# Kernel optimization log

Measured on AMD Instinct MI355X. Metric: run time of the kernel, lower is better.

The kernel has to match this reference:

```python
import jax, jax.numpy as jnp
import numpy as np

B, H, W, S, C = 16, 128, 128, 4, 64
SC = S * C
SK_ITERS, SK_EPS = 20, 1e-6


def setup_inputs() -> dict:
    key = jax.random.key(0)
    ks = jax.random.split(key, 12)
    x = jax.random.normal(ks[0], (B, H, W, S, C), dtype=jnp.float32)
    # torch Linear weights are [out, in], kaiming-uniform-ish scale ~ 1/sqrt(in)
    w_pre = jax.random.normal(ks[1], (S, SC), dtype=jnp.float32) / np.sqrt(SC)
    w_post = jax.random.normal(ks[2], (S, SC), dtype=jnp.float32) / np.sqrt(SC)
    w_res = jax.random.normal(ks[3], (S * S, SC), dtype=jnp.float32) / np.sqrt(SC)
    b_pre = jax.random.normal(ks[4], (1, S), dtype=jnp.float32) * 0.01
    b_res = jax.random.normal(ks[5], (S * S,), dtype=jnp.float32) * 0.01
    b_post = jax.random.normal(ks[6], (1, S), dtype=jnp.float32) * 0.01
    alpha_pre = jax.random.normal(ks[7], (1,), dtype=jnp.float32) * 0.01
    alpha_res = jax.random.normal(ks[8], (1,), dtype=jnp.float32) * 0.01
    alpha_post = jax.random.normal(ks[9], (1,), dtype=jnp.float32) * 0.01
    rms_w = jnp.ones((SC,), dtype=jnp.float32)
    # conv kernel HWIO for 3x3 same-padded Conv2d(C, C, bias=False)
    conv_w = jax.random.normal(ks[10], (3, 3, C, C), dtype=jnp.float32) / np.sqrt(9 * C)
    return {"x": x, "w_pre": w_pre, "w_post": w_post, "w_res": w_res,
            "b_pre": b_pre, "b_res": b_res, "b_post": b_post,
            "alpha_pre": alpha_pre, "alpha_res": alpha_res, "alpha_post": alpha_post,
            "rms_w": rms_w, "conv_w": conv_w}


def _sinkhorn(h_tilde):
    # h_tilde: [B,H,W,S,S]; stable softmax-style shift then 20 row/col rescales
    h = h_tilde - h_tilde.max(axis=(-2, -1), keepdims=True)
    h = jnp.exp(h)
    def body(_, h):
        h = h / (h.sum(axis=-2, keepdims=True) + SK_EPS)
        h = h / (h.sum(axis=-1, keepdims=True) + SK_EPS)
        return h
    return jax.lax.fori_loop(0, SK_ITERS, body, h)


def reference(x, w_pre, w_post, w_res, b_pre, b_res, b_post,
              alpha_pre, alpha_res, alpha_post, rms_w, conv_w):
    s = b_pre.shape[-1]
    x_arrow = x.reshape(*x.shape[:-2], -1)           # [B,H,W,S*C]
    eps = jnp.finfo(x.dtype).eps                     # torch RMSNorm default eps
    x_norm = x_arrow * jax.lax.rsqrt(jnp.mean(x_arrow * x_arrow, axis=-1, keepdims=True) + eps)
    x_norm = x_norm * rms_w

    h_tilde_pre = alpha_pre * (x_norm @ w_pre.T) + b_pre          # [B,H,W,S]
    h_tilde_post = alpha_post * (x_norm @ w_post.T) + b_post       # [B,H,W,S]
    h_tilde_res = alpha_res * (x_norm @ w_res.T).reshape(*x.shape[:-2], s, s) \
                  + b_res.reshape(s, s)                            # [B,H,W,S,S]

    h_pre = jax.nn.sigmoid(h_tilde_pre)                            # [B,H,W,S]
    h_res = _sinkhorn(h_tilde_res)                                 # [B,H,W,S,S]
    h_post = 2.0 * jax.nn.sigmoid(h_tilde_post)                    # [B,H,W,S]

    # x_pre = h_pre @ x (pre-mix across streams) -> [B,H,W,C]
    x_pre = jnp.einsum('bhws,bhwsc->bhwc', h_pre, x)
    # layer: Conv2d(C,C,3,padding=1,bias=False), applied in NHWC directly
    layer_out = jax.lax.conv_general_dilated(
        x_pre, conv_w, window_strides=(1, 1), padding='SAME',
        dimension_numbers=('NHWC', 'HWIO', 'NHWC'))                # [B,H,W,C]

    out = jnp.einsum('bhwst,bhwtc->bhwsc', h_res, x) \
          + h_post[..., :, None] * layer_out[..., None, :]         # [B,H,W,S,C]
    return out
```

## Files before the change

kernel.cpp:

```cpp
#include <hip/hip_runtime.h>
#include <cstdint>
#include <cstring>

typedef unsigned int u32;
typedef unsigned short u16;
typedef __attribute__((ext_vector_type(8))) __bf16 bf16x8;
typedef __attribute__((ext_vector_type(4))) float f32x4;

#define DEV static __device__ __forceinline__

DEV float bf2f(u16 v){ u32 u = ((u32)v)<<16; float f; __builtin_memcpy(&f,&u,4); return f; }
DEV u16 f2bf(float f){ u32 u; __builtin_memcpy(&u,&f,4); u32 r = u + 0x7fffu + ((u>>16)&1u); return (u16)(r>>16); }
DEV void unpk(u32 v, float& lo, float& hi){
  u32 a = v<<16; u32 b = v & 0xffff0000u;
  __builtin_memcpy(&lo,&a,4); __builtin_memcpy(&hi,&b,4);
}
DEV u32 pk2(float lo, float hi){ return (u32)f2bf(lo) | (((u32)f2bf(hi))<<16); }
DEV float fsigm(float x){ return __builtin_amdgcn_rcpf(1.f + __expf(-x)); }
DEV f32x4 MFMA16(uint4 a, uint4 b, f32x4 c){
  return __builtin_amdgcn_mfma_f32_16x16x32_bf16(
      __builtin_bit_cast(bf16x8, a), __builtin_bit_cast(bf16x8, b), c, 0, 0, 0);
}

DEV bool detect_bf16(const void* rmsw){ return ((const u16*)rmsw)[0] == 0x3F80u; }

DEV u32 rnd1(u32 f){ return (f + 0x7fffu + ((f>>16)&1u)) >> 16; }
DEV u32 rnd2(u32 lo, u32 hi){ return rnd1(lo) | (rnd1(hi)<<16); }

DEV uint4 load8(const void* p, size_t idx8, bool bf){
  if (bf) return ((const uint4*)p)[idx8];
  const uint4* q = (const uint4*)p;
  uint4 a = q[2*idx8], b = q[2*idx8+1];
  return make_uint4(rnd2(a.x,a.y), rnd2(a.z,a.w), rnd2(b.x,b.y), rnd2(b.z,b.w));
}
DEV void store8(void* p, size_t idx8, bool bf, const float* v){
  if (bf){
    ((uint4*)p)[idx8] = make_uint4(pk2(v[0],v[1]),pk2(v[2],v[3]),pk2(v[4],v[5]),pk2(v[6],v[7]));
  } else {
    float4* q = (float4*)p;
    q[2*idx8]   = make_float4(v[0],v[1],v[2],v[3]);
    q[2*idx8+1] = make_float4(v[4],v[5],v[6],v[7]);
  }
}
DEV float ldsc(const void* p, int i, bool bf){
  return bf ? bf2f(((const u16*)p)[i]) : ((const float*)p)[i];
}

__global__ __launch_bounds__(256) void prepack_kernel(
    const void* __restrict__ wpre, const void* __restrict__ wpost,
    const void* __restrict__ wres, const void* __restrict__ rmsw,
    const void* __restrict__ convw, u16* __restrict__ wsW, u16* __restrict__ wsC)
{
  const bool bf = detect_bf16(rmsw);
  int tid = blockIdx.x*256 + threadIdx.x;
  if (tid < 8192){
    int i = tid & 7, lane = (tid>>3)&63, nt = (tid>>9)&1, kk = tid>>10;
    int j = nt*16 + (lane&15);
    int k = kk*32 + ((lane>>4)<<3) + i;
    float v = 0.f;
    if (j < 4)       v = ldsc(wpre, j*256+k, bf);
    else if (j < 8)  v = ldsc(wpost, (j-4)*256+k, bf);
    else if (j < 24) v = ldsc(wres, (j-8)*256+k, bf);
    v *= ldsc(rmsw, k, bf);
    wsW[tid] = f2bf(v);
  }
  if (tid < 36864){
    int i = tid & 7, lane = (tid>>3)&63, nt = (tid>>9)&3, kk = tid>>11;
    int co = nt*16 + (lane&15);
    int k = kk*32 + ((lane>>4)<<3) + i;
    wsC[tid] = f2bf(ldsc(convw, k*64+co, bf));
  }
}

__global__ __launch_bounds__(256,2) void mHC_fused_kernel(
    const void* __restrict__ x,
    const void* __restrict__ bpre, const void* __restrict__ bres, const void* __restrict__ bpost,
    const void* __restrict__ apre, const void* __restrict__ ares, const void* __restrict__ apost,
    const void* __restrict__ rmsw,
    const u16* __restrict__ wsW, const u16* __restrict__ wsC,
    void* __restrict__ out)
{
  __shared__ __align__(16) u16 s_xpre[18*18*68];
  __shared__ __align__(16) u16 s_h[256*20];
  __shared__ __align__(16) u16 s_hpre[4][64];
  __shared__ __align__(16) u16 s_L[4][16*68];

  const bool bf = detect_bf16(rmsw);
  const int tid = threadIdx.x;
  const int wave = tid>>6, lane = tid&63;
  const int mm = lane&15, q = lane>>4;
  const int blk = blockIdx.x;
  const int bimg = blk>>6, ty = (blk>>3)&7, tx = blk&7;
  const size_t xb8 = (size_t)bimg*16384*32;
  const int gy0 = ty*16-1, gx0 = tx*16-1;

  const float a_pre = ldsc(apre,0,bf), a_res = ldsc(ares,0,bf), a_post = ldsc(apost,0,bf);
  const float al0 = (mm<4)? a_pre : (mm<8)? a_post : a_res;
  const float bi0 = (mm<4)? ldsc(bpre,mm,bf) : (mm<8)? ldsc(bpost,mm-4,bf) : ldsc(bres,mm-8,bf);
  const float al1 = a_res;
  const float bi1 = (mm<8)? ldsc(bres,mm+8,bf) : 0.f;

  const uint4* wWv = reinterpret_cast<const uint4*>(wsW);
  const uint4* wCv = reinterpret_cast<const uint4*>(wsC);

  for (int pass = wave; pass < 21; pass += 4){
    const int P  = pass*16 + mm;
    const int ey = P/18, ex = P - ey*18;
    const int gy = gy0+ey, gx = gx0+ex;
    const bool inimg = (P<324) && ((u32)gy < 128u) && ((u32)gx < 128u);
    const size_t p8 = xb8 + (size_t)(u32)(gy*128 + gx)*32;

    uint4 A[8];
    #pragma unroll
    for (int kk=0;kk<8;kk++){
      uint4 v = make_uint4(0u,0u,0u,0u);
      if (inimg) v = load8(x, p8 + kk*4+q, bf);
      A[kk] = v;
    }
    float ssq = 0.f;
    #pragma unroll
    for (int kk=0;kk<8;kk++){
      const u32 vv[4] = {A[kk].x,A[kk].y,A[kk].z,A[kk].w};
      #pragma unroll
      for (int w2=0;w2<4;w2++){ float lo,hi; unpk(vv[w2],lo,hi);
        ssq = __builtin_fmaf(lo,lo,ssq); ssq = __builtin_fmaf(hi,hi,ssq); }
    }
    ssq += __shfl_xor(ssq,16);
    ssq += __shfl_xor(ssq,32);
    const float scale = __builtin_amdgcn_rsqf(ssq*(1.f/256.f) + 1.1920928955078125e-07f);
    float rs[4];
    #pragma unroll
    for (int r=0;r<4;r++) rs[r] = __shfl(scale, q*4+r);

    f32x4 D0 = {0.f,0.f,0.f,0.f}, D1 = {0.f,0.f,0.f,0.f};
    #pragma unroll
    for (int kk=0;kk<8;kk++){
      D0 = MFMA16(A[kk], wWv[(kk*2+0)*64+lane], D0);
      D1 = MFMA16(A[kk], wWv[(kk*2+1)*64+lane], D1);
    }
    #pragma unroll
    for (int r=0;r<4;r++){
      const float ht0 = __builtin_fmaf(al0*rs[r], D0[r], bi0);
      const float ht1 = __builtin_fmaf(al1*rs[r], D1[r], bi1);
      const int Pr = pass*16 + q*4 + r;
      const int eyr = Pr/18, exr = Pr - eyr*18;
      if (mm < 4) s_hpre[wave][(q*4+r)*4+mm] = f2bf(fsigm(ht0));
      const bool intr = (Pr<324) && (eyr>=1) && (eyr<=16) && (exr>=1) && (exr<=16);
      if (intr){
        const int pid = (eyr-1)*16 + (exr-1);
        if (mm < 8) s_h[pid*20 + mm+8] = f2bf(ht1);
        else        s_h[pid*20 + mm-8] = f2bf(ht0);
        if (mm>=4 && mm<8) s_h[pid*20 + 12 + mm] = f2bf(2.f*fsigm(ht0));
      }
    }
    __builtin_amdgcn_wave_barrier();
    if (P < 324){
      float hp[4];
      { const uint2 hv = *reinterpret_cast<const uint2*>(&s_hpre[wave][mm*4]);
        unpk(hv.x, hp[0], hp[1]); unpk(hv.y, hp[2], hp[3]); }
      float xa[8] = {0,0,0,0,0,0,0,0}, xb[8] = {0,0,0,0,0,0,0,0};
      #pragma unroll
      for (int kk=0;kk<8;kk++){
        const float h = hp[kk>>1];
        const u32 vv[4] = {A[kk].x,A[kk].y,A[kk].z,A[kk].w};
        #pragma unroll
        for (int w2=0;w2<4;w2++){
          float lo,hi; unpk(vv[w2],lo,hi);
          if (kk&1){ xb[2*w2]  =__builtin_fmaf(h,lo,xb[2*w2]);  xb[2*w2+1]=__builtin_fmaf(h,hi,xb[2*w2+1]); }
          else     { xa[2*w2]  =__builtin_fmaf(h,lo,xa[2*w2]);  xa[2*w2+1]=__builtin_fmaf(h,hi,xa[2*w2+1]); }
        }
      }
      const int pix = ey*18+ex;
      uint2* dA = reinterpret_cast<uint2*>(&s_xpre[pix*68 + 8*q]);
      dA[0] = make_uint2(pk2(xa[0],xa[1]), pk2(xa[2],xa[3]));
      dA[1] = make_uint2(pk2(xa[4],xa[5]), pk2(xa[6],xa[7]));
      uint2* dB = reinterpret_cast<uint2*>(&s_xpre[pix*68 + 32 + 8*q]);
      dB[0] = make_uint2(pk2(xb[0],xb[1]), pk2(xb[2],xb[3]));
      dB[1] = make_uint2(pk2(xb[4],xb[5]), pk2(xb[6],xb[7]));
    }
    __builtin_amdgcn_wave_barrier();
  }
  __syncthreads();

  {
    const int p = tid;
    float h[16];
    const uint2* h2 = reinterpret_cast<const uint2*>(&s_h[p*20]);
    #pragma unroll
    for (int e=0;e<4;e++){ const uint2 v = h2[e];
      unpk(v.x,h[4*e],h[4*e+1]); unpk(v.y,h[4*e+2],h[4*e+3]); }
    float mx = h[0];
    #pragma unroll
    for (int e=1;e<16;e++) mx = fmaxf(mx,h[e]);
    #pragma unroll
    for (int e=0;e<16;e++) h[e] = __expf(h[e]-mx);
    for (int it=0; it<20; ++it){
      #pragma unroll
      for (int t=0;t<4;t++){
        const float rc = __builtin_amdgcn_rcpf((h[t]+h[4+t])+(h[8+t]+h[12+t]) + 1e-6f);
        h[t]*=rc; h[4+t]*=rc; h[8+t]*=rc; h[12+t]*=rc;
      }
      #pragma unroll
      for (int s=0;s<4;s++){
        const float rc = __builtin_amdgcn_rcpf((h[4*s]+h[4*s+1])+(h[4*s+2]+h[4*s+3]) + 1e-6f);
        h[4*s]*=rc; h[4*s+1]*=rc; h[4*s+2]*=rc; h[4*s+3]*=rc;
      }
    }
    uint2* hw = reinterpret_cast<uint2*>(&s_h[p*20]);
    #pragma unroll
    for (int e=0;e<4;e++) hw[e] = make_uint2(pk2(h[4*e],h[4*e+1]), pk2(h[4*e+2],h[4*e+3]));
  }
  __syncthreads();

  for (int i=0;i<4;i++){
    const int py = wave*4+i;
    f32x4 D[4];
    #pragma unroll
    for (int nt=0;nt<4;nt++) D[nt] = (f32x4){0.f,0.f,0.f,0.f};
    #pragma unroll
    for (int kk=0;kk<18;kk++){
      const int tq  = 4*kk+q;
      const int tap = tq>>3;
      const int ci0 = (tq&7)*8;
      const int dy = tap/3, dx = tap-3*dy;
      const int pix = (py+dy)*18 + (mm+dx);
      const uint2* a2 = reinterpret_cast<const uint2*>(&s_xpre[pix*68 + ci0]);
      const uint2 alo = a2[0], ahi = a2[1];
      const uint4 av = make_uint4(alo.x, alo.y, ahi.x, ahi.y);
      #pragma unroll
      for (int nt=0;nt<4;nt++)
        D[nt] = MFMA16(av, wCv[(kk*4+nt)*64+lane], D[nt]);
    }
    __builtin_amdgcn_wave_barrier();
    #pragma unroll
    for (int nt=0;nt<4;nt++)
      #pragma unroll
      for (int r=0;r<4;r++)
        s_L[wave][(q*4+r)*68 + nt*16 + mm] = f2bf(D[nt][r]);
    __builtin_amdgcn_wave_barrier();

    const int gy = ty*16+py, gx = tx*16+mm;
    const size_t p8 = xb8 + (size_t)(gy*128+gx)*32;
    uint4 A[8];
    #pragma unroll
    for (int kk=0;kk<8;kk++) A[kk] = load8(x, p8 + kk*4+q, bf);
    float xa[4][8], xb[4][8];
    #pragma unroll
    for (int t=0;t<4;t++){
      const u32 va[4] = {A[2*t].x,A[2*t].y,A[2*t].z,A[2*t].w};
      const u32 vb[4] = {A[2*t+1].x,A[2*t+1].y,A[2*t+1].z,A[2*t+1].w};
      #pragma unroll
      for (int w2=0;w2<4;w2++){
        unpk(va[w2], xa[t][2*w2], xa[t][2*w2+1]);
        unpk(vb[w2], xb[t][2*w2], xb[t][2*w2+1]);
      }
    }
    const int pid = py*16+mm;
    float hr[16], hpo[4];
    {
      const uint2* h2 = reinterpret_cast<const uint2*>(&s_h[pid*20]);
      #pragma unroll
      for (int e=0;e<4;e++){ const uint2 v = h2[e];
        unpk(v.x,hr[4*e],hr[4*e+1]); unpk(v.y,hr[4*e+2],hr[4*e+3]); }
      const uint2 v4 = h2[4];
      unpk(v4.x,hpo[0],hpo[1]); unpk(v4.y,hpo[2],hpo[3]);
    }
    float LA[8], LB[8];
    {
      const uint2* lA = reinterpret_cast<const uint2*>(&s_L[wave][mm*68 + 8*q]);
      const uint2* lB = reinterpret_cast<const uint2*>(&s_L[wave][mm*68 + 32 + 8*q]);
      const uint2 a0v=lA[0], a1v=lA[1], b0v=lB[0], b1v=lB[1];
      unpk(a0v.x,LA[0],LA[1]); unpk(a0v.y,LA[2],LA[3]);
      unpk(a1v.x,LA[4],LA[5]); unpk(a1v.y,LA[6],LA[7]);
      unpk(b0v.x,LB[0],LB[1]); unpk(b0v.y,LB[2],LB[3]);
      unpk(b1v.x,LB[4],LB[5]); unpk(b1v.y,LB[6],LB[7]);
    }
    const size_t ob8 = ((size_t)bimg*16384 + (size_t)(gy*128+gx))*32;
    #pragma unroll
    for (int s=0;s<4;s++){
      float oA[8], oB[8];
      #pragma unroll
      for (int j2=0;j2<8;j2++){ oA[j2]=hpo[s]*LA[j2]; oB[j2]=hpo[s]*LB[j2]; }
      #pragma unroll
      for (int t=0;t<4;t++){
        const float w0 = hr[4*s+t];
        #pragma unroll
        for (int j2=0;j2<8;j2++){
          oA[j2]=__builtin_fmaf(w0,xa[t][j2],oA[j2]);
          oB[j2]=__builtin_fmaf(w0,xb[t][j2],oB[j2]);
        }
      }
      store8(out, ob8 + s*8 + q,     bf, oA);
      store8(out, ob8 + s*8 + 4 + q, bf, oB);
    }
  }
}

extern "C" void kernel_launch(void* const* d_in, const int* in_sizes, int n_in,
                              void* d_out, int out_size, void* d_ws, size_t ws_size,
                              hipStream_t stream)
{
  const void* x     = d_in[0];
  const void* wpre  = d_in[1];
  const void* wpost = d_in[2];
  const void* wres  = d_in[3];
  const void* bpre  = d_in[4];
  const void* bres  = d_in[5];
  const void* bpost = d_in[6];
  const void* apre  = d_in[7];
  const void* ares  = d_in[8];
  const void* apost = d_in[9];
  const void* rmsw  = d_in[10];
  const void* convw = d_in[11];
  u16* wsW = (u16*)d_ws;
  u16* wsC = wsW + 8192;

  hipLaunchKernelGGL(prepack_kernel, dim3(144), dim3(256), 0, stream,
                     wpre, wpost, wres, rmsw, convw, wsW, wsC);
  hipLaunchKernelGGL(mHC_fused_kernel, dim3(1024), dim3(256), 0, stream,
                     x, bpre, bres, bpost, apre, ares, apost, rmsw, wsW, wsC, d_out);
}
```

Measured before the change: 709.5 us.

## Keep interior x tile in registers and split halo pass to skip redundant work

The first phase now loads each wave's 4 interior pixel rows of x into registers (128 VGPRs of uint4) and reuses them in the final output phase, so the second global read of x is removed. Halo pixels are handled in a separate pass that computes only the h_pre projection (one MFMA chain instead of two) and skips the res/post projections they never needed. The cost is heavy register pressure from holding Ax[4][8], which may lower occupancy or cause spills, and the final loop is now fully unrolled.

```diff
diff --git a/kernel.cpp b/kernel.cpp
--- a/kernel.cpp
+++ b/kernel.cpp
@@ -103,11 +103,90 @@
   const uint4* wWv = reinterpret_cast<const uint4*>(wsW);
   const uint4* wCv = reinterpret_cast<const uint4*>(wsC);
 
-  for (int pass = wave; pass < 21; pass += 4){
-    const int P  = pass*16 + mm;
-    const int ey = P/18, ex = P - ey*18;
+  uint4 Ax[4][8];
+  {
+    const int gx = tx*16 + mm;
+    #pragma unroll
+    for (int i=0;i<4;i++){
+      const int gy = ty*16 + wave*4 + i;
+      const size_t p8 = xb8 + (size_t)(gy*128 + gx)*32;
+      #pragma unroll
+      for (int kk=0;kk<8;kk++) Ax[i][kk] = load8(x, p8 + kk*4+q, bf);
+    }
+  }
+
+  #pragma unroll
+  for (int i=0;i<4;i++){
+    float ssq = 0.f;
+    #pragma unroll
+    for (int kk=0;kk<8;kk++){
+      const u32 vv[4] = {Ax[i][kk].x,Ax[i][kk].y,Ax[i][kk].z,Ax[i][kk].w};
+      #pragma unroll
+      for (int w2=0;w2<4;w2++){ float lo,hi; unpk(vv[w2],lo,hi);
+        ssq = __builtin_fmaf(lo,lo,ssq); ssq = __builtin_fmaf(hi,hi,ssq); }
+    }
+    ssq += __shfl_xor(ssq,16);
+    ssq += __shfl_xor(ssq,32);
+    const float scale = __builtin_amdgcn_rsqf(ssq*(1.f/256.f) + 1.1920928955078125e-07f);
+    float rs[4];
+    #pragma unroll
+    for (int r=0;r<4;r++) rs[r] = __shfl(scale, q*4+r);
+
+    f32x4 D0 = {0.f,0.f,0.f,0.f}, D1 = {0.f,0.f,0.f,0.f};
+    #pragma unroll
+    for (int kk=0;kk<8;kk++){
+      D0 = MFMA16(Ax[i][kk], wWv[(kk*2+0)*64+lane], D0);
+      D1 = MFMA16(Ax[i][kk], wWv[(kk*2+1)*64+lane], D1);
+    }
+    #pragma unroll
+    for (int r=0;r<4;r++){
+      const float ht0 = __builtin_fmaf(al0*rs[r], D0[r], bi0);
+      const float ht1 = __builtin_fmaf(al1*rs[r], D1[r], bi1);
+      if (mm < 4) s_hpre[wave][(q*4+r)*4+mm] = f2bf(fsigm(ht0));
+      const int pid = (wave*4+i)*16 + (q*4+r);
+      if (mm < 8) s_h[pid*20 + mm+8] = f2bf(ht1);
+      else        s_h[pid*20 + mm-8] = f2bf(ht0);
+      if (mm>=4 && mm<8) s_h[pid*20 + 12 + mm] = f2bf(2.f*fsigm(ht0));
+    }
+    __builtin_amdgcn_wave_barrier();
+    {
+      float hp[4];
+      { const uint2 hv = *reinterpret_cast<const uint2*>(&s_hpre[wave][mm*4]);
+        unpk(hv.x, hp[0], hp[1]); unpk(hv.y, hp[2], hp[3]); }
+      float xa[8] = {0,0,0,0,0,0,0,0}, xb[8] = {0,0,0,0,0,0,0,0};
+      #pragma unroll
+      for (int kk=0;kk<8;kk++){
+        const float h = hp[kk>>1];
+        const u32 vv[4] = {Ax[i][kk].x,Ax[i][kk].y,Ax[i][kk].z,Ax[i][kk].w};
+        #pragma unroll
+        for (int w2=0;w2<4;w2++){
+          float lo,hi; unpk(vv[w2],lo,hi);
+          if (kk&1){ xb[2*w2]  =__builtin_fmaf(h,lo,xb[2*w2]);  xb[2*w2+1]=__builtin_fmaf(h,hi,xb[2*w2+1]); }
+          else     { xa[2*w2]  =__builtin_fmaf(h,lo,xa[2*w2]);  xa[2*w2+1]=__builtin_fmaf(h,hi,xa[2*w2+1]); }
+        }
+      }
+      const int pix = (wave*4+i+1)*18 + (mm+1);
+      uint2* dA = reinterpret_cast<uint2*>(&s_xpre[pix*68 + 8*q]);
+      dA[0] = make_uint2(pk2(xa[0],xa[1]), pk2(xa[2],xa[3]));
+      dA[1] = make_uint2(pk2(xa[4],xa[5]), pk2(xa[6],xa[7]));
+      uint2* dB = reinterpret_cast<uint2*>(&s_xpre[pix*68 + 32 + 8*q]);
+      dB[0] = make_uint2(pk2(xb[0],xb[1]), pk2(xb[2],xb[3]));
+      dB[1] = make_uint2(pk2(xb[4],xb[5]), pk2(xb[6],xb[7]));
+    }
+    __builtin_amdgcn_wave_barrier();
+  }
+
+  #pragma unroll
+  for (int hp_=0; hp_<2; ++hp_){
+    const bool pv = hp_ ? (mm==0) : true;
+    const int hx = hp_ ? (64+wave) : (wave*16+mm);
+    int ey, ex;
+    if (hx < 18)      { ey = 0;       ex = hx;      }
+    else if (hx < 36) { ey = 17;      ex = hx-18;   }
+    else if (hx < 52) { ey = hx-35;   ex = 0;       }
+    else              { ey = hx-51;   ex = 17;      }
     const int gy = gy0+ey, gx = gx0+ex;
-    const bool inimg = (P<324) && ((u32)gy < 128u) && ((u32)gx < 128u);
+    const bool inimg = pv && ((u32)gy < 128u) && ((u32)gx < 128u);
     const size_t p8 = xb8 + (size_t)(u32)(gy*128 + gx)*32;
 
     uint4 A[8];
@@ -132,29 +211,19 @@
     #pragma unroll
     for (int r=0;r<4;r++) rs[r] = __shfl(scale, q*4+r);
 
-    f32x4 D0 = {0.f,0.f,0.f,0.f}, D1 = {0.f,0.f,0.f,0.f};
-    #pragma unroll
-    for (int kk=0;kk<8;kk++){
-      D0 = MFMA16(A[kk], wWv[(kk*2+0)*64+lane], D0);
-      D1 = MFMA16(A[kk], wWv[(kk*2+1)*64+lane], D1);
-    }
+    f32x4 D0 = {0.f,0.f,0.f,0.f};
+    #pragma unroll
+    for (int kk=0;kk<8;kk++) D0 = MFMA16(A[kk], wWv[(kk*2+0)*64+lane], D0);
+
     #pragma unroll
     for (int r=0;r<4;r++){
-      const float ht0 = __builtin_fmaf(al0*rs[r], D0[r], bi0);
-      const float ht1 = __builtin_fmaf(al1*rs[r], D1[r], bi1);
-      const int Pr = pass*16 + q*4 + r;
-      const int eyr = Pr/18, exr = Pr - eyr*18;
-      if (mm < 4) s_hpre[wave][(q*4+r)*4+mm] = f2bf(fsigm(ht0));
-      const bool intr = (Pr<324) && (eyr>=1) && (eyr<=16) && (exr>=1) && (exr<=16);
-      if (intr){
-        const int pid = (eyr-1)*16 + (exr-1);
-        if (mm < 8) s_h[pid*20 + mm+8] = f2bf(ht1);
-        else        s_h[pid*20 + mm-8] = f2bf(ht0);
-        if (mm>=4 && mm<8) s_h[pid*20 + 12 + mm] = f2bf(2.f*fsigm(ht0));
-      }
-    }
-    __builtin_amdgcn_wave_barrier();
-    if (P < 324){
+      if (mm < 4){
+        const float ht0 = __builtin_fmaf(al0*rs[r], D0[r], bi0);
+        s_hpre[wave][(q*4+r)*4+mm] = f2bf(fsigm(ht0));
+      }
+    }
+    __builtin_amdgcn_wave_barrier();
+    if (pv){
       float hp[4];
       { const uint2 hv = *reinterpret_cast<const uint2*>(&s_hpre[wave][mm*4]);
         unpk(hv.x, hp[0], hp[1]); unpk(hv.y, hp[2], hp[3]); }
@@ -170,7 +239,7 @@
           else     { xa[2*w2]  =__builtin_fmaf(h,lo,xa[2*w2]);  xa[2*w2+1]=__builtin_fmaf(h,hi,xa[2*w2+1]); }
         }
       }
-      const int pix = ey*18+ex;
+      const int pix = ey*18 + ex;
       uint2* dA = reinterpret_cast<uint2*>(&s_xpre[pix*68 + 8*q]);
       dA[0] = make_uint2(pk2(xa[0],xa[1]), pk2(xa[2],xa[3]));
       dA[1] = make_uint2(pk2(xa[4],xa[5]), pk2(xa[6],xa[7]));
@@ -212,6 +281,7 @@
   }
   __syncthreads();
 
+  #pragma unroll
   for (int i=0;i<4;i++){
     const int py = wave*4+i;
     f32x4 D[4];
@@ -240,15 +310,11 @@
     __builtin_amdgcn_wave_barrier();
 
     const int gy = ty*16+py, gx = tx*16+mm;
-    const size_t p8 = xb8 + (size_t)(gy*128+gx)*32;
-    uint4 A[8];
-    #pragma unroll
-    for (int kk=0;kk<8;kk++) A[kk] = load8(x, p8 + kk*4+q, bf);
     float xa[4][8], xb[4][8];
     #pragma unroll
     for (int t=0;t<4;t++){
-      const u32 va[4] = {A[2*t].x,A[2*t].y,A[2*t].z,A[2*t].w};
-      const u32 vb[4] = {A[2*t+1].x,A[2*t+1].y,A[2*t+1].z,A[2*t+1].w};
+      const u32 va[4] = {Ax[i][2*t].x,Ax[i][2*t].y,Ax[i][2*t].z,Ax[i][2*t].w};
+      const u32 vb[4] = {Ax[i][2*t+1].x,Ax[i][2*t+1].y,Ax[i][2*t+1].z,Ax[i][2*t+1].w};
       #pragma unroll
       for (int w2=0;w2<4;w2++){
         unpk(va[w2], xa[t][2*w2], xa[t][2*w2+1]);
```

Measured after the change: 698.0 us. Within noise of the previous version (-1.6%).
